# Kernel optimization log

Measured on AMD Instinct MI355X. Metric: run time of the kernel, lower is better.

## Reference

```python
import jax, jax.numpy as jnp
import numpy as np

D = 1024        # hidden_size
H = 16          # num_heads
HD = D // H     # head_dim = 64
K = 4           # conv kernel size
I = int(D * 2.7)  # ffn intermediate = 2764
B, T = 2, 2048
EPS = 1e-6
GATE_BIAS = 4.0


def setup_inputs() -> dict:
    key = jax.random.key(0)
    ks = jax.random.split(key, 16)
    s = D ** -0.5
    return {
        "x": jax.random.normal(ks[0], (B, T, D), jnp.float32),
        "norm1_w": jnp.ones((D,), jnp.float32),
        "norm2_w": jnp.ones((D,), jnp.float32),
        "conv_w": jax.random.normal(ks[1], (D, K), jnp.float32) * 0.2,
        "conv_b": jnp.zeros((D,), jnp.float32),
        "wq": jax.random.normal(ks[2], (D, D), jnp.float32) * s,
        "wk": jax.random.normal(ks[3], (D, D), jnp.float32) * s,
        "wv": jax.random.normal(ks[4], (D, D), jnp.float32) * s,
        "wb": jax.random.normal(ks[5], (D, H), jnp.float32) * s,
        "wa": jax.random.normal(ks[6], (D, H), jnp.float32) * s,
        "wo": jax.random.normal(ks[7], (D, D), jnp.float32) * s,
        "wg": jax.random.normal(ks[8], (D, I), jnp.float32) * s,
        "wu": jax.random.normal(ks[9], (D, I), jnp.float32) * s,
        "wd": jax.random.normal(ks[10], (I, D), jnp.float32) * (I ** -0.5),
    }


def _rmsnorm(x, w):
    return x * jax.lax.rsqrt(jnp.mean(x * x, axis=-1, keepdims=True) + EPS) * w


def _causal_depthwise_conv(x, conv_w, conv_b):
    # x: [B,T,D]; depthwise causal conv, kernel K, then SiLU
    xt = jnp.transpose(x, (0, 2, 1))  # [B,D,T]
    y = jax.lax.conv_general_dilated(
        xt, conv_w[:, None, :],  # [D,1,K]
        window_strides=(1,), padding=[(K - 1, 0)],
        feature_group_count=D,
        dimension_numbers=("NCH", "OIH", "NCH"))
    y = jnp.transpose(y, (0, 2, 1)) + conv_b  # [B,T,D]
    return jax.nn.silu(y)


def _l2norm(x):
    return x * jax.lax.rsqrt(jnp.sum(x * x, axis=-1, keepdims=True) + EPS)


def _gated_delta_rule(xc, wq, wk, wv, wb, wa):
    b, t = xc.shape[0], xc.shape[1]
    q = _l2norm((xc @ wq).reshape(b, t, H, HD))
    k = _l2norm((xc @ wk).reshape(b, t, H, HD))
    v = (xc @ wv).reshape(b, t, H, HD)
    beta = jax.nn.sigmoid(xc @ wb)              # [B,T,H]
    alpha = jax.nn.sigmoid(xc @ wa + GATE_BIAS)  # [B,T,H] decay gate

    # time-major for scan
    qt = jnp.moveaxis(q, 1, 0)
    kt = jnp.moveaxis(k, 1, 0)
    vt = jnp.moveaxis(v, 1, 0)
    bt = jnp.moveaxis(beta, 1, 0)
    at = jnp.moveaxis(alpha, 1, 0)

    S0 = jnp.zeros((b, H, HD, HD), xc.dtype)  # [B,H,dk,dv]

    def step(S, inp):
        q_, k_, v_, b_, a_ = inp
        S = a_[..., None, None] * S
        pred = jnp.einsum("bhkv,bhk->bhv", S, k_)
        S = S + k_[..., :, None] * (b_[..., None] * (v_ - pred))[..., None, :]
        o = jnp.einsum("bhkv,bhk->bhv", S, q_)
        return S, o

    _, o = jax.lax.scan(step, S0, (qt, kt, vt, bt, at))  # [T,B,H,HD]
    return jnp.moveaxis(o, 1, 0).reshape(b, t, D)


def reference(x, norm1_w, norm2_w, conv_w, conv_b, wq, wk, wv, wb, wa, wo,
              wg, wu, wd):
    residual = x
    xn = _rmsnorm(x, norm1_w)
    xc = _causal_depthwise_conv(xn, conv_w, conv_b)
    mixer_out = _gated_delta_rule(xc, wq, wk, wv, wb, wa) @ wo
    h = residual + mixer_out
    hn = _rmsnorm(h, norm2_w)
    ffn = (jax.nn.silu(hn @ wg) * (hn @ wu)) @ wd
    return h + ffn
```

## Files before the change

### kernel.cpp

```cpp
#include <hip/hip_runtime.h>
#include <math.h>

#define D_ 1024
#define H_ 16
#define HD_ 64
#define KW_ 4
#define I_ 2764
#define IP_ 2816
#define NQKV_ 3200
#define NGU_ 5632
#define B_ 2
#define T_ 2048
#define BT_ (B_*T_)
#define ND_ (BT_*D_)
#define NH_ (BT_*H_)
#define NCH_ 32
#define NG_ (32*NCH_)
#define EPS_ 1e-6f
#define GATE_BIAS_ 4.0f

typedef __attribute__((ext_vector_type(8))) short bf16x8;
typedef __attribute__((ext_vector_type(4))) float f32x4;

#define MFMA_(a,b,c) __builtin_amdgcn_mfma_f32_16x16x32_bf16(a, b, c, 0, 0, 0)
#define GLDS_(src, dst) __builtin_amdgcn_global_load_lds( \
    (const __attribute__((address_space(1))) void*)(src), \
    (__attribute__((address_space(3))) void*)(dst), 16, 0, 0)

__device__ float f_sc1[BT_];
__device__ float f_be[NH_];
__device__ float f_al[NH_];
__device__ float f_h[ND_];
__device__ float g_rs[NG_ * 256];
__device__ float g_BmT[(size_t)NG_*4096];
__device__ unsigned short g_Gqk[(size_t)NG_*4096];
__device__ unsigned short g_Y[(size_t)NG_*4096];
__device__ unsigned short g_ZT[(size_t)NG_*4096];
__device__ unsigned short g_A[(size_t)NG_*4096];
__device__ unsigned short g_S[(size_t)NG_*4096];
__device__ unsigned short b_q[ND_];
__device__ unsigned short b_k[ND_];
__device__ unsigned short b_v[ND_];
__device__ unsigned short b_xc[ND_];
__device__ unsigned short b_o[ND_];
__device__ unsigned short b_hn[ND_];
__device__ unsigned short b_f[(size_t)BT_*IP_];
__device__ unsigned short b_wqkvT[(size_t)NQKV_*D_];
__device__ unsigned short b_woT[D_*D_];
__device__ unsigned short b_wguT[(size_t)NGU_*D_];
__device__ unsigned short b_wdT[(size_t)D_*IP_];

__device__ __forceinline__ unsigned short f2b(float x) {
  union { float f; unsigned u; } a; a.f = x;
  unsigned r = a.u + 0x7fff + ((a.u >> 16) & 1);
  return (unsigned short)(r >> 16);
}
__device__ __forceinline__ float b2f(unsigned short s) {
  union { unsigned u; float f; } a; a.u = ((unsigned)s) << 16; return a.f;
}

__device__ __forceinline__ const unsigned short* bsel(int id) {
  switch (id) {
    case 0: return b_xc;  case 1: return b_o;    case 2: return b_hn;
    case 3: return b_f;   case 4: return b_wqkvT; case 5: return b_woT;
    case 6: return b_wguT; default: return b_wdT;
  }
}
__device__ __forceinline__ unsigned short* bselw(int id) {
  return (unsigned short*)bsel(id);
}

__global__ __launch_bounds__(256) void rmssc_k(const float* __restrict__ x) {
  int row = blockIdx.x;
  int tid = threadIdx.x;
  float4 v = ((const float4*)(x + (size_t)row * D_))[tid];
  float ss = v.x*v.x + v.y*v.y + v.z*v.z + v.w*v.w;
  #pragma unroll
  for (int o = 32; o > 0; o >>= 1) ss += __shfl_down(ss, o);
  __shared__ float sred[4];
  if ((tid & 63) == 0) sred[tid >> 6] = ss;
  __syncthreads();
  if (tid == 0)
    f_sc1[row] = rsqrtf((sred[0]+sred[1]+sred[2]+sred[3]) / (float)D_ + EPS_);
}

__global__ __launch_bounds__(256) void rms2_k(const float* __restrict__ w) {
  int row = blockIdx.x;
  const float* xr = f_h + (size_t)row * D_;
  int tid = threadIdx.x;
  float4 v = ((const float4*)xr)[tid];
  float ss = v.x*v.x + v.y*v.y + v.z*v.z + v.w*v.w;
  #pragma unroll
  for (int o = 32; o > 0; o >>= 1) ss += __shfl_down(ss, o);
  __shared__ float sred[4];
  __shared__ float sscale;
  if ((tid & 63) == 0) sred[tid >> 6] = ss;
  __syncthreads();
  if (tid == 0)
    sscale = rsqrtf((sred[0]+sred[1]+sred[2]+sred[3]) / (float)D_ + EPS_);
  __syncthreads();
  float s = sscale;
  float4 wv = ((const float4*)w)[tid];
  unsigned short* orow = b_hn + (size_t)row * D_ + tid * 4;
  orow[0] = f2b(v.x*s*wv.x); orow[1] = f2b(v.y*s*wv.y);
  orow[2] = f2b(v.z*s*wv.z); orow[3] = f2b(v.w*s*wv.w);
}

__global__ __launch_bounds__(256) void conv2_k(const float* __restrict__ x,
                                               const float* __restrict__ cw,
                                               const float* __restrict__ cb,
                                               const float* __restrict__ n1w) {
  int idx = blockIdx.x * 256 + threadIdx.x;
  int d = idx & (D_ - 1);
  int bt = idx >> 10;
  int t = bt & (T_ - 1);
  float wd = n1w[d];
  float acc = cb[d];
  #pragma unroll
  for (int j = 0; j < KW_; j++) {
    int tt = t - (KW_ - 1) + j;
    if (tt >= 0) {
      int off = j - (KW_ - 1);
      acc += x[(size_t)idx + (size_t)off * D_] * f_sc1[bt + off] * wd * cw[d * KW_ + j];
    }
  }
  float s = acc / (1.f + expf(-acc));
  b_xc[idx] = f2b(s);
}

__global__ __launch_bounds__(256) void castTqkv_k(const float* __restrict__ wq,
                                                  const float* __restrict__ wk,
                                                  const float* __restrict__ wv,
                                                  const float* __restrict__ wb,
                                                  const float* __restrict__ wa) {
  __shared__ float s[64][65];
  int n0 = blockIdx.x * 64, k0 = blockIdx.y * 64;
  int tx = threadIdx.x & 63, ty = threadIdx.x >> 6;
  int nn = n0 + tx;
  const float* src = nullptr; int col = 0, ld = 1024;
  if (nn < 1024)      { src = wq; col = nn; }
  else if (nn < 2048) { src = wk; col = nn - 1024; }
  else if (nn < 3072) { src = wv; col = nn - 2048; }
  else if (nn < 3088) { src = wb; col = nn - 3072; ld = 16; }
  else if (nn < 3104) { src = wa; col = nn - 3088; ld = 16; }
  #pragma unroll
  for (int j = ty; j < 64; j += 4)
    s[j][tx] = src ? src[(size_t)(k0 + j) * ld + col] : 0.f;
  __syncthreads();
  #pragma unroll
  for (int j = ty; j < 64; j += 4)
    b_wqkvT[(size_t)(n0 + j) * D_ + k0 + tx] = f2b(s[tx][j]);
}

__global__ __launch_bounds__(256) void castTgu_k(const float* __restrict__ wg,
                                                 const float* __restrict__ wu) {
  __shared__ float s[64][65];
  int n0 = blockIdx.x * 64, k0 = blockIdx.y * 64;
  int tx = threadIdx.x & 63, ty = threadIdx.x >> 6;
  int nn = n0 + tx;
  int inner = nn & 31;
  int col = (nn >> 5) * 16 + (inner & 15);
  const float* src = (inner < 16) ? wg : wu;
  bool ok = (col < I_);
  #pragma unroll
  for (int j = ty; j < 64; j += 4)
    s[j][tx] = ok ? src[(size_t)(k0 + j) * I_ + col] : 0.f;
  __syncthreads();
  #pragma unroll
  for (int j = ty; j < 64; j += 4)
    b_wguT[(size_t)(n0 + j) * D_ + k0 + tx] = f2b(s[tx][j]);
}

__global__ __launch_bounds__(256) void castT_k(const float* __restrict__ W,
                                               int K, int N, int outid, int Kp) {
  __shared__ float s[64][65];
  unsigned short* out = bselw(outid);
  int k0 = blockIdx.y * 64, n0 = blockIdx.x * 64;
  int tx = threadIdx.x & 63, ty = threadIdx.x >> 6;
  #pragma unroll
  for (int j = ty; j < 64; j += 4) {
    int kk = k0 + j, nn = n0 + tx;
    s[j][tx] = (kk < K && nn < N) ? W[(size_t)kk * N + nn] : 0.f;
  }
  __syncthreads();
  #pragma unroll
  for (int j = ty; j < 64; j += 4)
    out[(size_t)(n0 + j) * Kp + k0 + tx] = f2b(s[tx][j]);
}

__global__ __launch_bounds__(256) void gemm_bf16(int aid, int bid, int Kp, int mode,
                                                 const float* __restrict__ ext,
                                                 float* __restrict__ eout) {
  __shared__ __align__(16) unsigned short Al[2][128 * 32];
  __shared__ __align__(16) unsigned short Bl[2][128 * 32];
  const unsigned short* A = bsel(aid);
  const unsigned short* Bt = bsel(bid);
  int tid = threadIdx.x;
  int nbx = gridDim.x;
  int nwg = nbx * gridDim.y;
  int lid = blockIdx.y * nbx + blockIdx.x;
  int cpx = nwg >> 3;
  int swzb = (lid & 7) * cpx + (lid >> 3);
  int m0 = (swzb / nbx) * 128, n0 = (swzb % nbx) * 128;
  int wave = tid >> 6, lane = tid & 63;
  int wm = (wave >> 1) * 64, wn = (wave & 1) * 64;
  int lrow = tid >> 2;
  int lcol = ((tid & 3) ^ ((lrow >> 1) & 3)) * 8;
  f32x4 acc[4][4] = {};
  const int l15 = lane & 15, lg = lane >> 4;
  const int sw = (lg ^ ((l15 >> 1) & 3)) * 8;
  const int nt = Kp >> 5;
  {
    const unsigned short* Ag = A + (size_t)m0 * Kp;
    const unsigned short* Bg = Bt + (size_t)n0 * Kp;
    GLDS_(Ag + (size_t)lrow * Kp + lcol,        Al[0] + wave * 512);
    GLDS_(Ag + (size_t)(64 + lrow) * Kp + lcol, Al[0] + 2048 + wave * 512);
    GLDS_(Bg + (size_t)lrow * Kp + lcol,        Bl[0] + wave * 512);
    GLDS_(Bg + (size_t)(64 + lrow) * Kp + lcol, Bl[0] + 2048 + wave * 512);
  }
  __syncthreads();
  for (int t = 0; t < nt; t++) {
    int cur = t & 1;
    if (t + 1 < nt) {
      int k0 = (t + 1) << 5;
      const unsigned short* Ag = A + (size_t)m0 * Kp + k0;
      const unsigned short* Bg = Bt + (size_t)n0 * Kp + k0;
      GLDS_(Ag + (size_t)lrow * Kp + lcol,        Al[cur ^ 1] + wave * 512);
      GLDS_(Ag + (size_t)(64 + lrow) * Kp + lcol, Al[cur ^ 1] + 2048 + wave * 512);
      GLDS_(Bg + (size_t)lrow * Kp + lcol,        Bl[cur ^ 1] + wave * 512);
      GLDS_(Bg + (size_t)(64 + lrow) * Kp + lcol, Bl[cur ^ 1] + 2048 + wave * 512);
    }
    bf16x8 af[4], bf[4];
    #pragma unroll
    for (int i = 0; i < 4; i++)
      af[i] = *(const bf16x8*)&Al[cur][(wm + i * 16 + l15) * 32 + sw];
    #pragma unroll
    for (int j = 0; j < 4; j++)
      bf[j] = *(const bf16x8*)&Bl[cur][(wn + j * 16 + l15) * 32 + sw];
    #pragma unroll
    for (int i = 0; i < 4; i++)
      #pragma unroll
      for (int j = 0; j < 4; j++)
        acc[i][j] = MFMA_(af[i], bf[j], acc[i][j]);
    __syncthreads();
  }
  int C0 = n0 + wn;
  if (mode == 0) {
    if (C0 < 2048) {
      unsigned short* dst = (C0 < 1024) ? b_q : b_k;
      int cbase = C0 & 1023;
      #pragma unroll
      for (int i = 0; i < 4; i++) {
        int r0i = m0 + wm + i * 16 + lg * 4;
        #pragma unroll
        for (int r = 0; r < 4; r++) {
          float ss = acc[i][0][r]*acc[i][0][r] + acc[i][1][r]*acc[i][1][r]
                   + acc[i][2][r]*acc[i][2][r] + acc[i][3][r]*acc[i][3][r];
          ss += __shfl_xor(ss, 1); ss += __shfl_xor(ss, 2);
          ss += __shfl_xor(ss, 4); ss += __shfl_xor(ss, 8);
          float sc = rsqrtf(ss + EPS_);
          #pragma unroll
          for (int j = 0; j < 4; j++)
            dst[(size_t)(r0i + r) * D_ + cbase + j * 16 + l15] = f2b(acc[i][j][r] * sc);
        }
      }
    } else if (C0 < 3072) {
      int cbase = C0 & 1023;
      #pragma unroll
      for (int i = 0; i < 4; i++) {
        int r0i = m0 + wm + i * 16 + lg * 4;
        #pragma unroll
        for (int j = 0; j < 4; j++)
          #pragma unroll
          for (int r = 0; r < 4; r++)
            b_v[(size_t)(r0i + r) * D_ + cbase + j * 16 + l15] = f2b(acc[i][j][r]);
      }
    } else if (C0 == 3072) {
      #pragma unroll
      for (int i = 0; i < 4; i++) {
        int r0i = m0 + wm + i * 16 + lg * 4;
        #pragma unroll
        for (int r = 0; r < 4; r++) {
          float vb = acc[i][0][r];
          f_be[(size_t)(r0i + r) * H_ + l15] = 1.f / (1.f + expf(-vb));
          float va = acc[i][1][r] + GATE_BIAS_;
          f_al[(size_t)(r0i + r) * H_ + l15] = 1.f / (1.f + expf(-va));
        }
      }
    }
  } else if (mode == 1) {
    #pragma unroll
    for (int i = 0; i < 4; i++) {
      int r0i = m0 + wm + i * 16 + lg * 4;
      #pragma unroll
      for (int jp = 0; jp < 2; jp++) {
        int j = jp * 2;
        int Lbase = ((C0 + j * 16) >> 5) * 16;
        #pragma unroll
        for (int r = 0; r < 4; r++) {
          float g = acc[i][j][r], u = acc[i][j + 1][r];
          float sg = g / (1.f + expf(-g));
          b_f[(size_t)(r0i + r) * IP_ + Lbase + l15] = f2b(sg * u);
        }
      }
    }
  } else if (mode == 2) {
    #pragma unroll
    for (int i = 0; i < 4; i++) {
      int r0i = m0 + wm + i * 16 + lg * 4;
      #pragma unroll
      for (int j = 0; j < 4; j++)
        #pragma unroll
        for (int r = 0; r < 4; r++) {
          size_t off = (size_t)(r0i + r) * D_ + C0 + j * 16 + l15;
          f_h[off] = ext[off] + acc[i][j][r];
        }
    }
  } else {
    #pragma unroll
    for (int i = 0; i < 4; i++) {
      int r0i = m0 + wm + i * 16 + lg * 4;
      #pragma unroll
      for (int j = 0; j < 4; j++)
        #pragma unroll
        for (int r = 0; r < 4; r++) {
          size_t off = (size_t)(r0i + r) * D_ + C0 + j * 16 + l15;
          eout[off] = f_h[off] + acc[i][j][r];
        }
    }
  }
}


__global__ __launch_bounds__(256) void prep_k() {
  __shared__ __align__(16) char sm[46608];
  unsigned short* sKT = (unsigned short*)sm;
  unsigned short* sVT = (unsigned short*)(sm + 10240);
  unsigned short* sAb16 = (unsigned short*)(sm + 20480);
  float* sX  = (float*)(sm + 28928);
  unsigned short* sYT = (unsigned short*)(sm + 28928);
  float* sL  = (float*)(sm + 45568);
  float* sB  = (float*)(sm + 45824);
  float* sS2 = (float*)(sm + 46080);
  float* sDec= (float*)(sm + 46336);
  float* sGC = (float*)(sm + 46592);

  int gid = blockIdx.x;
  int ch = gid & 31, bh = gid >> 5;
  int b = bh >> 4, h = bh & 15;
  int c0 = ch * 64, hb = h * HD_;
  int rowb = b * T_ + c0;
  int tid = threadIdx.x;
  int w = tid >> 6, lane = tid & 63, l15 = lane & 15, lg = lane >> 4;
  size_t g4 = (size_t)gid * 4096;

  if (tid < 64) {
    size_t rb = ((size_t)(rowb + tid)) * H_ + h;
    float la = log2f(f_al[rb]);
    #pragma unroll
    for (int m = 1; m < 64; m <<= 1) {
      float o = __shfl_up(la, m);
      if (tid >= m) la += o;
    }
    float L63 = __shfl(la, 63);
    float bt = f_be[rb];
    float g = exp2f(la);
    sL[tid] = la; sB[tid] = bt; sS2[tid] = bt * g;
    sDec[tid] = exp2f(L63 - la);
    if (tid == 63) sGC[0] = g;
    g_rs[(size_t)gid*256 + tid*4 + 0] = bt;
    g_rs[(size_t)gid*256 + tid*4 + 1] = bt * g;
    g_rs[(size_t)gid*256 + tid*4 + 2] = g;
  }
  __syncthreads();

  {
    int tp = tid >> 3, q8 = tid & 7;
    int t0 = 2 * tp, t1 = 2 * tp + 1;
    const bf16x8 k0 = *(const bf16x8*)(b_k + (size_t)(rowb + t0) * D_ + hb + q8 * 8);
    const bf16x8 k1 = *(const bf16x8*)(b_k + (size_t)(rowb + t1) * D_ + hb + q8 * 8);
    const bf16x8 v0 = *(const bf16x8*)(b_v + (size_t)(rowb + t0) * D_ + hb + q8 * 8);
    const bf16x8 v1 = *(const bf16x8*)(b_v + (size_t)(rowb + t1) * D_ + hb + q8 * 8);
    float s0 = sB[t0], s1v = sB[t1];
    unsigned* KT32 = (unsigned*)sKT;
    unsigned* VT32 = (unsigned*)sVT;
    #pragma unroll
    for (int i = 0; i < 8; i++) {
      int k = q8 * 8 + i;
      KT32[k*40 + tp] = (unsigned)(unsigned short)k0[i] |
                        ((unsigned)(unsigned short)k1[i] << 16);
      unsigned lo = f2b(b2f((unsigned short)v0[i]) * s0);
      unsigned hi = f2b(b2f((unsigned short)v1[i]) * s1v);
      VT32[k*40 + tp] = lo | (hi << 16);
    }
  }
  {
    bf16x8 bK[2], aK[4][2], aQ[4][2];
    #pragma unroll
    for (int k2 = 0; k2 < 2; k2++) {
      bK[k2] = *(const bf16x8*)&b_k[(size_t)(rowb + w*16 + l15)*D_ + hb + k2*32 + lg*8];
      #pragma unroll
      for (int ti = 0; ti < 4; ti++) {
        aK[ti][k2] = *(const bf16x8*)&b_k[(size_t)(rowb + ti*16 + l15)*D_ + hb + k2*32 + lg*8];
        aQ[ti][k2] = *(const bf16x8*)&b_q[(size_t)(rowb + ti*16 + l15)*D_ + hb + k2*32 + lg*8];
      }
    }
    f32x4 ck[4] = {}, cq[4] = {};
    #pragma unroll
    for (int k2 = 0; k2 < 2; k2++)
      #pragma unroll
      for (int ti = 0; ti < 4; ti++) {
        ck[ti] = MFMA_(aK[ti][k2], bK[k2], ck[ti]);
        cq[ti] = MFMA_(aQ[ti][k2], bK[k2], cq[ti]);
      }
    int j = w*16 + l15;
    float Lj = sL[j];
    #pragma unroll
    for (int ti = 0; ti < 4; ti++)
      #pragma unroll
      for (int r = 0; r < 4; r++) {
        int t = ti*16 + lg*4 + r;
        float ratio = exp2f(sL[t] - Lj);
        sAb16[t*66 + j] = f2b((j < t) ? sB[t] * ratio * ck[ti][r] : 0.f);
        g_Gqk[g4 + t*64 + j] = f2b((j <= t) ? ratio * cq[ti][r] : 0.f);
      }
  }
  __syncthreads();
  {
    int c = tid >> 2, p = tid & 3;
    for (int t = 0; t < 64; t++) {
      float s = 0.f;
      for (int jj = p; jj < t; jj += 4)
        s += b2f(sAb16[t*66 + jj]) * sX[jj*65 + c];
      s += __shfl_xor(s, 1);
      s += __shfl_xor(s, 2);
      float xv = ((t == c) ? 1.f : 0.f) - s;
      if (p == 0) sX[t*65 + c] = xv;
    }
  }
  __syncthreads();
  int m0 = w * 16;
  f32x4 cyT[4], cz[4];
  {
    bf16x8 aKT[2];
    aKT[0] = *(const bf16x8*)&sKT[(m0 + l15)*80 + lg*8];
    aKT[1] = *(const bf16x8*)&sKT[(m0 + l15)*80 + 32 + lg*8];
    #pragma unroll
    for (int n = 0; n < 4; n++) {
      cyT[n] = f32x4{0.f, 0.f, 0.f, 0.f};
      #pragma unroll
      for (int k2 = 0; k2 < 2; k2++) {
        bf16x8 bb;
        #pragma unroll
        for (int i = 0; i < 8; i++) {
          int tp = k2*32 + lg*8 + i;
          bb[i] = (short)f2b(sX[(n*16 + l15)*65 + tp] * sS2[tp]);
        }
        cyT[n] = MFMA_(aKT[k2], bb, cyT[n]);
      }
    }
    bf16x8 aT2[2];
    #pragma unroll
    for (int k2 = 0; k2 < 2; k2++)
      #pragma unroll
      for (int i = 0; i < 8; i++) {
        int tp = k2*32 + lg*8 + i;
        aT2[k2][i] = (short)f2b(sX[(m0 + l15)*65 + tp] * sS2[tp]);
      }
    #pragma unroll
    for (int n = 0; n < 4; n++) {
      f32x4 c = {};
      #pragma unroll
      for (int k2 = 0; k2 < 2; k2++) {
        bf16x8 bKT = *(const bf16x8*)&sKT[(n*16 + l15)*80 + k2*32 + lg*8];
        c = MFMA_(aT2[k2], bKT, c);
      }
      #pragma unroll
      for (int r = 0; r < 4; r++)
        g_Y[g4 + (m0 + lg*4 + r)*64 + n*16 + l15] = f2b(c[r]);
    }
    bf16x8 aV[2];
    aV[0] = *(const bf16x8*)&sVT[(m0 + l15)*80 + lg*8];
    aV[1] = *(const bf16x8*)&sVT[(m0 + l15)*80 + 32 + lg*8];
    #pragma unroll
    for (int n = 0; n < 4; n++) {
      cz[n] = f32x4{0.f, 0.f, 0.f, 0.f};
      #pragma unroll
      for (int k2 = 0; k2 < 2; k2++) {
        bf16x8 bT;
        #pragma unroll
        for (int i = 0; i < 8; i++)
          bT[i] = (short)f2b(sX[(n*16 + l15)*65 + k2*32 + lg*8 + i]);
        cz[n] = MFMA_(aV[k2], bT, cz[n]);
      }
      #pragma unroll
      for (int r = 0; r < 4; r++)
        g_ZT[g4 + (m0 + lg*4 + r)*64 + n*16 + l15] = f2b(cz[n][r]);
    }
  }
  __syncthreads();
  #pragma unroll
  for (int n = 0; n < 4; n++)
    #pragma unroll
    for (int r = 0; r < 4; r++) {
      sYT[(m0 + lg*4 + r)*88 + n*16 + l15] = f2b(cyT[n][r]);
      sVT[(m0 + lg*4 + r)*80 + n*16 + l15] = f2b(cz[n][r]);
    }
  {
    int xx = tid >> 2, q = tid & 3;
    bf16x8 v0 = *(const bf16x8*)&sKT[xx*80 + q*16];
    bf16x8 v1 = *(const bf16x8*)&sKT[xx*80 + q*16 + 8];
    bf16x8 d0, d1;
    #pragma unroll
    for (int i = 0; i < 8; i++) {
      d0[i] = (short)f2b(b2f((unsigned short)v0[i]) * sDec[q*16 + i]);
      d1[i] = (short)f2b(b2f((unsigned short)v1[i]) * sDec[q*16 + 8 + i]);
    }
    *(bf16x8*)&sKT[xx*80 + q*16] = d0;
    *(bf16x8*)&sKT[xx*80 + q*16 + 8] = d1;
  }
  __syncthreads();
  {
    float gC = sGC[0];
    bf16x8 aKd[2];
    aKd[0] = *(const bf16x8*)&sKT[(m0 + l15)*80 + lg*8];
    aKd[1] = *(const bf16x8*)&sKT[(m0 + l15)*80 + 32 + lg*8];
    #pragma unroll
    for (int n = 0; n < 4; n++) {
      f32x4 c = {};
      #pragma unroll
      for (int k2 = 0; k2 < 2; k2++) {
        bf16x8 bY = *(const bf16x8*)&sYT[(n*16 + l15)*88 + k2*32 + lg*8];
        c = MFMA_(aKd[k2], bY, c);
      }
      #pragma unroll
      for (int r = 0; r < 4; r++) {
        int row = m0 + lg*4 + r, col = n*16 + l15;
        g_A[g4 + row*64 + col] = f2b(((row == col) ? gC : 0.f) - c[r]);
      }
    }
    #pragma unroll
    for (int n = 0; n < 4; n++) {
      f32x4 c = {};
      #pragma unroll
      for (int k2 = 0; k2 < 2; k2++) {
        bf16x8 bZ = *(const bf16x8*)&sVT[(n*16 + l15)*80 + k2*32 + lg*8];
        c = MFMA_(aKd[k2], bZ, c);
      }
      *(f32x4*)&g_BmT[g4 + (size_t)(n*16 + l15)*64 + m0 + lg*4] = c;
    }
  }
}

__global__ __launch_bounds__(256) void seq_k() {
  __shared__ __align__(16) unsigned short sST[4][16*80];
  int bh = blockIdx.x;
  int tid = threadIdx.x, w = tid >> 6, lane = tid & 63;
  int l15 = lane & 15, lg = lane >> 4;
  unsigned short* st = sST[w];
  for (int i = lane; i < 16*80; i += 64) st[i] = 0;
  f32x4 cerr[4] = {};
  bf16x8 aA[4][2];
  f32x4 cini[4];
  size_t g40 = (size_t)(bh * 32) * 4096;
  #pragma unroll
  for (int m = 0; m < 4; m++) {
    aA[m][0] = *(const bf16x8*)&g_A[g40 + (m*16 + l15)*64 + lg*8];
    aA[m][1] = *(const bf16x8*)&g_A[g40 + (m*16 + l15)*64 + 32 + lg*8];
    cini[m] = *(const f32x4*)&g_BmT[g40 + (w*16 + l15)*64 + m*16 + lg*4];
  }
  for (int ch = 0; ch < NCH_; ch++) {
    size_t gid = (size_t)bh * 32 + ch;
    float gC = g_rs[gid*256 + 254];
    bf16x8 bS0 = *(const bf16x8*)&st[l15*80 + lg*8];
    bf16x8 bS1 = *(const bf16x8*)&st[l15*80 + 32 + lg*8];
    *(bf16x8*)&g_S[gid*4096 + (w*16 + l15)*64 + lg*8] = bS0;
    *(bf16x8*)&g_S[gid*4096 + (w*16 + l15)*64 + 32 + lg*8] = bS1;
    bf16x8 aAn[4][2];
    f32x4 cin2[4];
    if (ch + 1 < NCH_) {
      size_t g4n = (gid + 1) * 4096;
      #pragma unroll
      for (int m = 0; m < 4; m++) {
        aAn[m][0] = *(const bf16x8*)&g_A[g4n + (m*16 + l15)*64 + lg*8];
        aAn[m][1] = *(const bf16x8*)&g_A[g4n + (m*16 + l15)*64 + 32 + lg*8];
        cin2[m] = *(const f32x4*)&g_BmT[g4n + (w*16 + l15)*64 + m*16 + lg*4];
      }
    }
    f32x4 c[4];
    #pragma unroll
    for (int m = 0; m < 4; m++) {
      #pragma unroll
      for (int r = 0; r < 4; r++)
        c[m][r] = cini[m][r] + gC * cerr[m][r];
      c[m] = MFMA_(aA[m][0], bS0, c[m]);
      c[m] = MFMA_(aA[m][1], bS1, c[m]);
    }
    #pragma unroll
    for (int m = 0; m < 4; m++)
      #pragma unroll
      for (int r = 0; r < 4; r++) {
        float x = c[m][r];
        unsigned short q = f2b(x);
        cerr[m][r] = x - b2f(q);
        st[l15*80 + m*16 + lg*4 + r] = q;
      }
    if (ch + 1 < NCH_) {
      #pragma unroll
      for (int m = 0; m < 4; m++) {
        aA[m][0] = aAn[m][0]; aA[m][1] = aAn[m][1];
        cini[m] = cin2[m];
      }
    }
  }
}

__global__ __launch_bounds__(256) void apply_k() {
  __shared__ __align__(16) unsigned short sUT[4][16*80];
  int gid = blockIdx.x;
  int ch = gid & 31, bh = gid >> 5;
  int b = bh >> 4, h = bh & 15;
  int c0 = ch * 64, hb = h * HD_;
  int rowb = b * T_ + c0;
  int tid = threadIdx.x, w = tid >> 6, lane = tid & 63;
  int l15 = lane & 15, lg = lane >> 4;
  unsigned short* ut = sUT[w];
  size_t g4 = (size_t)gid * 4096;
  bf16x8 aS[2];
  aS[0] = *(const bf16x8*)&g_S[g4 + (w*16 + l15)*64 + lg*8];
  aS[1] = *(const bf16x8*)&g_S[g4 + (w*16 + l15)*64 + 32 + lg*8];
  f32x4 cu[4];
  #pragma unroll
  for (int n = 0; n < 4; n++) {
    cu[n] = f32x4{0.f, 0.f, 0.f, 0.f};
    #pragma unroll
    for (int k2 = 0; k2 < 2; k2++) {
      bf16x8 bY = *(const bf16x8*)&g_Y[g4 + (n*16 + l15)*64 + k2*32 + lg*8];
      cu[n] = MFMA_(aS[k2], bY, cu[n]);
    }
  }
  #pragma unroll
  for (int n = 0; n < 4; n++)
    #pragma unroll
    for (int r = 0; r < 4; r++) {
      float zt = b2f(g_ZT[g4 + (w*16 + lg*4 + r)*64 + n*16 + l15]);
      ut[(lg*4 + r)*80 + n*16 + l15] = f2b(zt - cu[n][r]);
    }
  bf16x8 aU[2];
  aU[0] = *(const bf16x8*)&ut[l15*80 + lg*8];
  aU[1] = *(const bf16x8*)&ut[l15*80 + 32 + lg*8];
  f32x4 co[4];
  #pragma unroll
  for (int n = 0; n < 4; n++) {
    co[n] = f32x4{0.f, 0.f, 0.f, 0.f};
    #pragma unroll
    for (int k2 = 0; k2 < 2; k2++) {
      bf16x8 bQ = *(const bf16x8*)&b_q[(size_t)(rowb + n*16 + l15)*D_ + hb + k2*32 + lg*8];
      co[n] = MFMA_(aS[k2], bQ, co[n]);
    }
    float gm = g_rs[(size_t)gid*256 + (n*16 + l15)*4 + 2];
    #pragma unroll
    for (int r = 0; r < 4; r++) co[n][r] *= gm;
    #pragma unroll
    for (int k2 = 0; k2 < 2; k2++) {
      bf16x8 bG = *(const bf16x8*)&g_Gqk[g4 + (n*16 + l15)*64 + k2*32 + lg*8];
      co[n] = MFMA_(aU[k2], bG, co[n]);
    }
    ushort4 pk;
    pk.x = f2b(co[n][0]); pk.y = f2b(co[n][1]);
    pk.z = f2b(co[n][2]); pk.w = f2b(co[n][3]);
    *(ushort4*)&b_o[(size_t)(rowb + n*16 + l15)*D_ + hb + w*16 + lg*4] = pk;
  }
}

extern "C" void kernel_launch(void* const* d_in, const int* in_sizes, int n_in,
                              void* d_out, int out_size, void* d_ws, size_t ws_size,
                              hipStream_t stream) {
  const float* x   = (const float*)d_in[0];
  const float* n1w = (const float*)d_in[1];
  const float* n2w = (const float*)d_in[2];
  const float* cw  = (const float*)d_in[3];
  const float* cb  = (const float*)d_in[4];
  const float* wq  = (const float*)d_in[5];
  const float* wk  = (const float*)d_in[6];
  const float* wv  = (const float*)d_in[7];
  const float* wb  = (const float*)d_in[8];
  const float* wa  = (const float*)d_in[9];
  const float* wo  = (const float*)d_in[10];
  const float* wg  = (const float*)d_in[11];
  const float* wu  = (const float*)d_in[12];
  const float* wd  = (const float*)d_in[13];
  float* out = (float*)d_out;

  castTqkv_k<<<dim3(50, 16), 256, 0, stream>>>(wq, wk, wv, wb, wa);
  castT_k<<<dim3(16, 16), 256, 0, stream>>>(wo, D_, D_, 5, D_);
  castTgu_k<<<dim3(88, 16), 256, 0, stream>>>(wg, wu);
  castT_k<<<dim3(16, 44), 256, 0, stream>>>(wd, I_, D_, 7, IP_);

  rmssc_k<<<BT_, 256, 0, stream>>>(x);
  conv2_k<<<ND_ / 256, 256, 0, stream>>>(x, cw, cb, n1w);

  gemm_bf16<<<dim3(25, 32), 256, 0, stream>>>(0, 4, D_, 0, nullptr, nullptr);

  prep_k<<<NG_, 256, 0, stream>>>();
  seq_k<<<32, 256, 0, stream>>>();
  apply_k<<<NG_, 256, 0, stream>>>();

  gemm_bf16<<<dim3(8, 32), 256, 0, stream>>>(1, 5, D_, 2, x, nullptr);
  rms2_k<<<BT_, 256, 0, stream>>>(n2w);
  gemm_bf16<<<dim3(44, 32), 256, 0, stream>>>(2, 6, D_, 1, nullptr, nullptr);
  gemm_bf16<<<dim3(8, 32), 256, 0, stream>>>(3, 7, IP_, 3, nullptr, out);
}
```

Baseline: 502.5 us.

## Blocked register-resident triangular solve in prep_k with bf16 sX staging

Replaces the row-by-row forward substitution in prep_k, which did 64 sequential steps each reading shared memory, with a 4-row blocked solve. Each thread keeps its column's solved values in registers and reads A rows as 16-byte vectors, then writes the result once as bf16 into a padded shared buffer. This cuts shared-memory traffic and serial dependency depth in the inverse computation. Later stages now read the bf16 X buffer, so one fp32-to-bf16 rounding happens earlier, and the smaller LDS footprint may allow more blocks per CU.

```diff
diff --git a/kernel.cpp b/kernel.cpp
--- a/kernel.cpp
+++ b/kernel.cpp
@@ -333,17 +333,17 @@
 
 
 __global__ __launch_bounds__(256) void prep_k() {
-  __shared__ __align__(16) char sm[46608];
+  __shared__ __align__(16) char sm[40448];
   unsigned short* sKT = (unsigned short*)sm;
   unsigned short* sVT = (unsigned short*)(sm + 10240);
-  unsigned short* sAb16 = (unsigned short*)(sm + 20480);
-  float* sX  = (float*)(sm + 28928);
-  unsigned short* sYT = (unsigned short*)(sm + 28928);
-  float* sL  = (float*)(sm + 45568);
-  float* sB  = (float*)(sm + 45824);
-  float* sS2 = (float*)(sm + 46080);
-  float* sDec= (float*)(sm + 46336);
-  float* sGC = (float*)(sm + 46592);
+  unsigned short* sAb = (unsigned short*)(sm + 20480);
+  unsigned short* sYT = (unsigned short*)(sm + 20480);
+  unsigned short* sXb = (unsigned short*)(sm + 29696);
+  float* sL  = (float*)(sm + 38912);
+  float* sB  = (float*)(sm + 39168);
+  float* sS2 = (float*)(sm + 39424);
+  float* sDec= (float*)(sm + 39680);
+  float* sGC = (float*)(sm + 39936);
 
   int gid = blockIdx.x;
   int ch = gid & 31, bh = gid >> 5;
@@ -421,22 +421,65 @@
       for (int r = 0; r < 4; r++) {
         int t = ti*16 + lg*4 + r;
         float ratio = exp2f(sL[t] - Lj);
-        sAb16[t*66 + j] = f2b((j < t) ? sB[t] * ratio * ck[ti][r] : 0.f);
+        sAb[t*72 + j] = f2b((j < t) ? sB[t] * ratio * ck[ti][r] : 0.f);
         g_Gqk[g4 + t*64 + j] = f2b((j <= t) ? ratio * cq[ti][r] : 0.f);
       }
   }
   __syncthreads();
   {
-    int c = tid >> 2, p = tid & 3;
-    for (int t = 0; t < 64; t++) {
-      float s = 0.f;
-      for (int jj = p; jj < t; jj += 4)
-        s += b2f(sAb16[t*66 + jj]) * sX[jj*65 + c];
-      s += __shfl_xor(s, 1);
-      s += __shfl_xor(s, 2);
-      float xv = ((t == c) ? 1.f : 0.f) - s;
-      if (p == 0) sX[t*65 + c] = xv;
-    }
+    int c = (w << 4) + (lane >> 2);
+    int p = lane & 3;
+    int rb16 = p << 4;
+    float xr[16];
+    #pragma unroll
+    for (int j = 0; j < 16; j++) xr[j] = 0.f;
+    #pragma unroll
+    for (int q = 0; q < 16; q++) {
+      int r0 = 4 * q;
+      const unsigned short* abr = sAb + r0 * 72 + rb16;
+      bf16x8 A0a = *(const bf16x8*)(abr);
+      bf16x8 A0b = *(const bf16x8*)(abr + 8);
+      bf16x8 A1a = *(const bf16x8*)(abr + 72);
+      bf16x8 A1b = *(const bf16x8*)(abr + 80);
+      bf16x8 A2a = *(const bf16x8*)(abr + 144);
+      bf16x8 A2b = *(const bf16x8*)(abr + 152);
+      bf16x8 A3a = *(const bf16x8*)(abr + 216);
+      bf16x8 A3b = *(const bf16x8*)(abr + 224);
+      float s0 = 0.f, s1 = 0.f, s2 = 0.f, s3 = 0.f;
+      #pragma unroll
+      for (int j = 0; j < 8; j++) {
+        float xv = xr[j], xw = xr[8 + j];
+        s0 = fmaf(b2f((unsigned short)A0a[j]), xv, s0);
+        s1 = fmaf(b2f((unsigned short)A1a[j]), xv, s1);
+        s2 = fmaf(b2f((unsigned short)A2a[j]), xv, s2);
+        s3 = fmaf(b2f((unsigned short)A3a[j]), xv, s3);
+        s0 = fmaf(b2f((unsigned short)A0b[j]), xw, s0);
+        s1 = fmaf(b2f((unsigned short)A1b[j]), xw, s1);
+        s2 = fmaf(b2f((unsigned short)A2b[j]), xw, s2);
+        s3 = fmaf(b2f((unsigned short)A3b[j]), xw, s3);
+      }
+      s0 += __shfl_xor(s0, 1); s0 += __shfl_xor(s0, 2);
+      s1 += __shfl_xor(s1, 1); s1 += __shfl_xor(s1, 2);
+      s2 += __shfl_xor(s2, 1); s2 += __shfl_xor(s2, 2);
+      s3 += __shfl_xor(s3, 1); s3 += __shfl_xor(s3, 2);
+      float a10 = b2f(sAb[(r0+1)*72 + r0]);
+      float a20 = b2f(sAb[(r0+2)*72 + r0]);
+      float a21 = b2f(sAb[(r0+2)*72 + r0+1]);
+      float a30 = b2f(sAb[(r0+3)*72 + r0]);
+      float a31 = b2f(sAb[(r0+3)*72 + r0+1]);
+      float a32 = b2f(sAb[(r0+3)*72 + r0+2]);
+      float x0 = ((r0+0) == c ? 1.f : 0.f) - s0;
+      float x1 = ((r0+1) == c ? 1.f : 0.f) - s1 - a10*x0;
+      float x2 = ((r0+2) == c ? 1.f : 0.f) - s2 - a20*x0 - a21*x1;
+      float x3 = ((r0+3) == c ? 1.f : 0.f) - s3 - a30*x0 - a31*x1 - a32*x2;
+      if (p == (q >> 2)) {
+        int ji = 4 * (q & 3);
+        xr[ji+0] = x0; xr[ji+1] = x1; xr[ji+2] = x2; xr[ji+3] = x3;
+      }
+    }
+    #pragma unroll
+    for (int j = 0; j < 16; j++)
+      sXb[(rb16 + j)*72 + c] = f2b(xr[j]);
   }
   __syncthreads();
   int m0 = w * 16;
@@ -454,7 +497,7 @@
         #pragma unroll
         for (int i = 0; i < 8; i++) {
           int tp = k2*32 + lg*8 + i;
-          bb[i] = (short)f2b(sX[(n*16 + l15)*65 + tp] * sS2[tp]);
+          bb[i] = (short)f2b(b2f(sXb[(n*16 + l15)*72 + tp]) * sS2[tp]);
         }
         cyT[n] = MFMA_(aKT[k2], bb, cyT[n]);
       }
@@ -465,7 +508,7 @@
       #pragma unroll
       for (int i = 0; i < 8; i++) {
         int tp = k2*32 + lg*8 + i;
-        aT2[k2][i] = (short)f2b(sX[(m0 + l15)*65 + tp] * sS2[tp]);
+        aT2[k2][i] = (short)f2b(b2f(sXb[(m0 + l15)*72 + tp]) * sS2[tp]);
       }
     #pragma unroll
     for (int n = 0; n < 4; n++) {
@@ -487,10 +530,7 @@
       cz[n] = f32x4{0.f, 0.f, 0.f, 0.f};
       #pragma unroll
       for (int k2 = 0; k2 < 2; k2++) {
-        bf16x8 bT;
-        #pragma unroll
-        for (int i = 0; i < 8; i++)
-          bT[i] = (short)f2b(sX[(n*16 + l15)*65 + k2*32 + lg*8 + i]);
+        bf16x8 bT = *(const bf16x8*)&sXb[(n*16 + l15)*72 + k2*32 + lg*8];
         cz[n] = MFMA_(aV[k2], bT, cz[n]);
       }
       #pragma unroll
@@ -503,7 +543,7 @@
   for (int n = 0; n < 4; n++)
     #pragma unroll
     for (int r = 0; r < 4; r++) {
-      sYT[(m0 + lg*4 + r)*88 + n*16 + l15] = f2b(cyT[n][r]);
+      sYT[(m0 + lg*4 + r)*72 + n*16 + l15] = f2b(cyT[n][r]);
       sVT[(m0 + lg*4 + r)*80 + n*16 + l15] = f2b(cz[n][r]);
     }
   {
@@ -530,7 +570,7 @@
       f32x4 c = {};
       #pragma unroll
       for (int k2 = 0; k2 < 2; k2++) {
-        bf16x8 bY = *(const bf16x8*)&sYT[(n*16 + l15)*88 + k2*32 + lg*8];
+        bf16x8 bY = *(const bf16x8*)&sYT[(n*16 + l15)*72 + k2*32 + lg*8];
         c = MFMA_(aKd[k2], bY, c);
       }
       #pragma unroll
```

Result: faster. 464.0 us (-7.6%).
